# Kernel optimization log

Hardware: AMD Instinct MI355X
Metric: run time of the kernel (lower is better)

Reference implementation:

```python
import jax, jax.numpy as jnp
import numpy as np

N_NODES = 50000
N_EDGES = 1600000
N_GRAPHS = 500
BN_EPS = 1e-5


def gcn_conv(x, src, dst, W, b, n):
    # PyG GCNConv: add self-loops, symmetric normalization, scatter-add at target.
    xw = x @ W  # [N, out]
    deg = jax.ops.segment_sum(jnp.ones_like(dst, dtype=xw.dtype), dst, num_segments=n)
    dinv = jnp.where(deg > 0, jax.lax.rsqrt(deg), 0.0)
    coef = dinv[src] * dinv[dst]  # [E+N]
    out = jax.ops.segment_sum(xw[src] * coef[:, None], dst, num_segments=n)
    return out + b


def batchnorm(h, gamma, beta):
    # training-mode batch stats over the node dim (dropout omitted: eval)
    m = h.mean(axis=0)
    v = h.var(axis=0)
    return (h - m) * jax.lax.rsqrt(v + BN_EPS) * gamma + beta


def setup_inputs() -> dict:
    key = jax.random.key(0)
    ks = jax.random.split(key, 12)
    x = jax.random.normal(ks[0], (N_NODES, 64), dtype=jnp.float32)
    edge_index = jax.random.randint(ks[1], (2, N_EDGES), 0, N_NODES, dtype=jnp.int64)
    batch = jnp.sort(jax.random.randint(ks[2], (N_NODES,), 0, N_GRAPHS, dtype=jnp.int64))
    def glorot(k, shape):
        lim = float(np.sqrt(6.0 / (shape[0] + shape[1])))
        return jax.random.uniform(k, shape, jnp.float32, -lim, lim)
    return {
        "x": x, "edge_index": edge_index, "batch": batch,
        "W1": glorot(ks[3], (64, 128)), "b1": jnp.zeros((128,), jnp.float32),
        "gamma1": jnp.ones((128,), jnp.float32), "beta1": jnp.zeros((128,), jnp.float32),
        "W2": glorot(ks[4], (128, 128)), "b2": jnp.zeros((128,), jnp.float32),
        "gamma2": jnp.ones((128,), jnp.float32), "beta2": jnp.zeros((128,), jnp.float32),
        "W3": glorot(ks[5], (128, 256)), "b3": jnp.zeros((256,), jnp.float32),
        "gamma3": jnp.ones((256,), jnp.float32), "beta3": jnp.zeros((256,), jnp.float32),
        "W4": glorot(ks[6], (256, 10)), "b4": jnp.zeros((10,), jnp.float32),
    }


def reference(x, edge_index, batch, W1, b1, gamma1, beta1, W2, b2, gamma2, beta2,
              W3, b3, gamma3, beta3, W4, b4):
    n = x.shape[0]
    sl = jnp.arange(n, dtype=edge_index.dtype)
    src = jnp.concatenate([edge_index[0], sl])
    dst = jnp.concatenate([edge_index[1], sl])

    h = x
    for W, b, g, bt in ((W1, b1, gamma1, beta1), (W2, b2, gamma2, beta2)):
        h = gcn_conv(h, src, dst, W, b, n)
        h = jax.nn.relu(batchnorm(h, g, bt))

    # global mean pool over graphs
    sums = jax.ops.segment_sum(h, batch, num_segments=N_GRAPHS)
    cnts = jax.ops.segment_sum(jnp.ones((n,), h.dtype), batch, num_segments=N_GRAPHS)
    pooled = sums / jnp.maximum(cnts, 1.0)[:, None]  # [G, 128]

    # MLP head
    z = pooled @ W3 + b3
    z = jax.nn.relu(batchnorm(z, gamma3, beta3))
    return z @ W4 + b4  # [G, num_classes]
```

## Files before the change

kernel.cpp:

```cpp
#include <hip/hip_runtime.h>
#include <hip/hip_bf16.h>

#define BN_EPS 1e-5
#define PB 256

typedef __attribute__((ext_vector_type(8))) short short8;
typedef __attribute__((ext_vector_type(4))) float floatx4;


__device__ __forceinline__ unsigned short f2bf(float f) {
    union { float f; unsigned u; } v; v.f = f;
    unsigned r = v.u + 0x7FFF + ((v.u >> 16) & 1);
    return (unsigned short)(r >> 16);
}
__device__ __forceinline__ float bf2f(unsigned short h) {
    union { unsigned u; float f; } v; v.u = ((unsigned)h) << 16;
    return v.f;
}
__device__ __forceinline__ float lo16(unsigned u) { return bf2f((unsigned short)(u & 0xffff)); }
__device__ __forceinline__ float hi16(unsigned u) { return bf2f((unsigned short)(u >> 16)); }


__global__ void scan1_kernel(const int* __restrict__ in, int* __restrict__ part,
                             int* __restrict__ bsum, int n) {
    __shared__ int s[1024];
    int t = threadIdx.x;
    int i = blockIdx.x * 1024 + t;
    int v = (i < n) ? in[i] : 0;
    s[t] = v;
    __syncthreads();
    for (int off = 1; off < 1024; off <<= 1) {
        int x = (t >= off) ? s[t - off] : 0;
        __syncthreads();
        s[t] += x;
        __syncthreads();
    }
    if (i < n) part[i] = s[t] - v;
    if (t == 1023) bsum[blockIdx.x] = s[1023];
}

__global__ void scan2_kernel(int* __restrict__ bsum, int nb) {
    __shared__ int s[64];
    int t = threadIdx.x;
    int v = (t < nb) ? bsum[t] : 0;
    s[t] = v;
    __syncthreads();
    for (int off = 1; off < 64; off <<= 1) {
        int x = (t >= off) ? s[t - off] : 0;
        __syncthreads();
        s[t] += x;
        __syncthreads();
    }
    if (t < nb) bsum[t] = s[t] - v;
}

__global__ void scan3_rowptr(int* __restrict__ rowptr, const int* __restrict__ bsum,
                             int n, int E) {
    int i = blockIdx.x * blockDim.x + threadIdx.x;
    if (i < n) rowptr[i] += bsum[i >> 10];
    if (i == 0) rowptr[n] = E;
}

__global__ void scan3_add(int* __restrict__ arr, const int* __restrict__ bsum, int n) {
    int i = blockIdx.x * blockDim.x + threadIdx.x;
    if (i < n) arr[i] += bsum[i >> 10];
}


__global__ void hist_kernel(const int* __restrict__ dst, int* __restrict__ hist,
                            int E, int cpb, int NB) {
    __shared__ int h[256];
    int t = threadIdx.x;
    if (t < NB) h[t] = 0;
    __syncthreads();
    int base = blockIdx.x * cpb;
    int end = base + cpb; if (end > E) end = E;
    int e = base + t * 4;
    for (; e + 3 < end; e += 1024) {
        int4 d = *(const int4*)(dst + e);
        atomicAdd(&h[d.x >> 8], 1);
        atomicAdd(&h[d.y >> 8], 1);
        atomicAdd(&h[d.z >> 8], 1);
        atomicAdd(&h[d.w >> 8], 1);
    }
    for (; e < end; ++e) atomicAdd(&h[dst[e] >> 8], 1);
    __syncthreads();
    if (t < NB) hist[t * PB + blockIdx.x] = h[t];
}

__global__ void scatter_kernel(const int* __restrict__ src, const int* __restrict__ dst,
                               const int* __restrict__ offs, unsigned* __restrict__ part,
                               int E, int cpb, int NB) {
    __shared__ int cur[256];
    int t = threadIdx.x;
    if (t < NB) cur[t] = offs[t * PB + blockIdx.x];
    __syncthreads();
    int base = blockIdx.x * cpb;
    int end = base + cpb; if (end > E) end = E;
    int e = base + t * 4;
    for (; e + 3 < end; e += 1024) {
        int4 d4 = *(const int4*)(dst + e);
        int4 s4 = *(const int4*)(src + e);
        int dd[4] = {d4.x, d4.y, d4.z, d4.w};
        int sv[4] = {s4.x, s4.y, s4.z, s4.w};
#pragma unroll
        for (int i = 0; i < 4; ++i) {
            int pos = atomicAdd(&cur[dd[i] >> 8], 1);
            part[pos] = ((unsigned)sv[i] << 8) | (unsigned)(dd[i] & 255);
        }
    }
    for (; e < end; ++e) {
        int d = dst[e];
        int pos = atomicAdd(&cur[d >> 8], 1);
        part[pos] = ((unsigned)src[e] << 8) | (unsigned)(d & 255);
    }
}

__global__ void bucket_count(const unsigned* __restrict__ part, const int* __restrict__ offs,
                             int* __restrict__ cnt, float* __restrict__ dinv,
                             int E, int N, int NB) {
    __shared__ int cw[256];
    int b = blockIdx.x;
    int t = threadIdx.x;
    cw[t] = 0;
    __syncthreads();
    int bstart = offs[b * PB];
    int bend = (b + 1 < NB) ? offs[(b + 1) * PB] : E;
    for (int e = bstart + t; e < bend; e += 256)
        atomicAdd(&cw[part[e] & 255u], 1);
    __syncthreads();
    int node = (b << 8) + t;
    if (node < N) {
        int c = cw[t];
        cnt[node] = c;
        dinv[node] = rsqrtf((float)(c + 1));
    }
}

__global__ void bucket_fill(const unsigned* __restrict__ part, const int* __restrict__ offs,
                            const int* __restrict__ rowptr, int* __restrict__ csr,
                            int E, int N, int NB) {
    __shared__ int cur[256];
    int b = blockIdx.x;
    int t = threadIdx.x;
    int node = (b << 8) + t;
    cur[t] = (node < N) ? rowptr[node] : 0;
    __syncthreads();
    int bstart = offs[b * PB];
    int bend = (b + 1 < NB) ? offs[(b + 1) * PB] : E;
    for (int e = bstart + t; e < bend; e += 256) {
        unsigned pr = part[e];
        int pos = atomicAdd(&cur[pr & 255u], 1);
        csr[pos] = (int)(pr >> 8);
    }
}


__global__ void prescale64_bf(const float* __restrict__ x, const float* __restrict__ dinv,
                              unsigned short* __restrict__ y, int N) {
    int t = blockIdx.x * blockDim.x + threadIdx.x;
    int total = N * 8;
    if (t >= total) return;
    int r = t >> 3;
    float d = dinv[r];
    float4 a = ((const float4*)x)[t * 2];
    float4 b = ((const float4*)x)[t * 2 + 1];
    uint4 o;
    o.x = (unsigned)f2bf(a.x * d) | ((unsigned)f2bf(a.y * d) << 16);
    o.y = (unsigned)f2bf(a.z * d) | ((unsigned)f2bf(a.w * d) << 16);
    o.z = (unsigned)f2bf(b.x * d) | ((unsigned)f2bf(b.y * d) << 16);
    o.w = (unsigned)f2bf(b.z * d) | ((unsigned)f2bf(b.w * d) << 16);
    ((uint4*)y)[t] = o;
}

__global__ __launch_bounds__(256) void agg64_bf(
    const unsigned short* __restrict__ y, const int* __restrict__ rowptr,
    const int* __restrict__ csr, const float* __restrict__ dinv,
    unsigned short* __restrict__ A16, int N) {
    int wv = (blockIdx.x * blockDim.x + threadIdx.x) >> 6;
    int lane = threadIdx.x & 63;
    int node = wv * 2 + (lane >> 5);
    if (node >= N) return;
    int cu = lane & 31;
    const unsigned* yp = (const unsigned*)y;
    unsigned v = yp[(size_t)node * 32 + cu];
    float a0 = lo16(v), a1 = hi16(v);
    int b = rowptr[node], e = rowptr[node + 1];
    int i = b;
    for (; i + 7 < e; i += 8) {
        int s0 = csr[i], s1 = csr[i + 1], s2 = csr[i + 2], s3 = csr[i + 3];
        int s4 = csr[i + 4], s5 = csr[i + 5], s6 = csr[i + 6], s7 = csr[i + 7];
        unsigned v0 = yp[(size_t)s0 * 32 + cu];
        unsigned v1 = yp[(size_t)s1 * 32 + cu];
        unsigned v2 = yp[(size_t)s2 * 32 + cu];
        unsigned v3 = yp[(size_t)s3 * 32 + cu];
        unsigned v4 = yp[(size_t)s4 * 32 + cu];
        unsigned v5 = yp[(size_t)s5 * 32 + cu];
        unsigned v6 = yp[(size_t)s6 * 32 + cu];
        unsigned v7 = yp[(size_t)s7 * 32 + cu];
        a0 += ((lo16(v0) + lo16(v1)) + (lo16(v2) + lo16(v3)))
            + ((lo16(v4) + lo16(v5)) + (lo16(v6) + lo16(v7)));
        a1 += ((hi16(v0) + hi16(v1)) + (hi16(v2) + hi16(v3)))
            + ((hi16(v4) + hi16(v5)) + (hi16(v6) + hi16(v7)));
    }
    for (; i + 3 < e; i += 4) {
        int s0 = csr[i], s1 = csr[i + 1], s2 = csr[i + 2], s3 = csr[i + 3];
        unsigned v0 = yp[(size_t)s0 * 32 + cu];
        unsigned v1 = yp[(size_t)s1 * 32 + cu];
        unsigned v2 = yp[(size_t)s2 * 32 + cu];
        unsigned v3 = yp[(size_t)s3 * 32 + cu];
        a0 += (lo16(v0) + lo16(v1)) + (lo16(v2) + lo16(v3));
        a1 += (hi16(v0) + hi16(v1)) + (hi16(v2) + hi16(v3));
    }
    for (; i < e; ++i) {
        unsigned v0 = yp[(size_t)csr[i] * 32 + cu];
        a0 += lo16(v0);
        a1 += hi16(v0);
    }
    float d = dinv[node];
    ((unsigned*)A16)[(size_t)node * 32 + cu] =
        (unsigned)f2bf(a0 * d) | ((unsigned)f2bf(a1 * d) << 16);
}

__global__ __launch_bounds__(256) void agg128_bf(
    const unsigned short* __restrict__ y, const int* __restrict__ rowptr,
    const int* __restrict__ csr, const float* __restrict__ dinv,
    unsigned short* __restrict__ A16, int N) {
    int wv = (blockIdx.x * blockDim.x + threadIdx.x) >> 6;
    int lane = threadIdx.x & 63;
    int node = wv * 2 + (lane >> 5);
    if (node >= N) return;
    int c2 = lane & 31;
    const uint2* yp = (const uint2*)y;
    uint2 v = yp[(size_t)node * 32 + c2];
    float a0 = lo16(v.x), a1 = hi16(v.x), a2 = lo16(v.y), a3 = hi16(v.y);
    int b = rowptr[node], e = rowptr[node + 1];
    int i = b;
    for (; i + 7 < e; i += 8) {
        int s0 = csr[i], s1 = csr[i + 1], s2 = csr[i + 2], s3 = csr[i + 3];
        int s4 = csr[i + 4], s5 = csr[i + 5], s6 = csr[i + 6], s7 = csr[i + 7];
        uint2 v0 = yp[(size_t)s0 * 32 + c2];
        uint2 v1 = yp[(size_t)s1 * 32 + c2];
        uint2 v2 = yp[(size_t)s2 * 32 + c2];
        uint2 v3 = yp[(size_t)s3 * 32 + c2];
        uint2 v4 = yp[(size_t)s4 * 32 + c2];
        uint2 v5 = yp[(size_t)s5 * 32 + c2];
        uint2 v6 = yp[(size_t)s6 * 32 + c2];
        uint2 v7 = yp[(size_t)s7 * 32 + c2];
        a0 += ((lo16(v0.x) + lo16(v1.x)) + (lo16(v2.x) + lo16(v3.x)))
            + ((lo16(v4.x) + lo16(v5.x)) + (lo16(v6.x) + lo16(v7.x)));
        a1 += ((hi16(v0.x) + hi16(v1.x)) + (hi16(v2.x) + hi16(v3.x)))
            + ((hi16(v4.x) + hi16(v5.x)) + (hi16(v6.x) + hi16(v7.x)));
        a2 += ((lo16(v0.y) + lo16(v1.y)) + (lo16(v2.y) + lo16(v3.y)))
            + ((lo16(v4.y) + lo16(v5.y)) + (lo16(v6.y) + lo16(v7.y)));
        a3 += ((hi16(v0.y) + hi16(v1.y)) + (hi16(v2.y) + hi16(v3.y)))
            + ((hi16(v4.y) + hi16(v5.y)) + (hi16(v6.y) + hi16(v7.y)));
    }
    for (; i + 3 < e; i += 4) {
        int s0 = csr[i], s1 = csr[i + 1], s2 = csr[i + 2], s3 = csr[i + 3];
        uint2 v0 = yp[(size_t)s0 * 32 + c2];
        uint2 v1 = yp[(size_t)s1 * 32 + c2];
        uint2 v2 = yp[(size_t)s2 * 32 + c2];
        uint2 v3 = yp[(size_t)s3 * 32 + c2];
        a0 += (lo16(v0.x) + lo16(v1.x)) + (lo16(v2.x) + lo16(v3.x));
        a1 += (hi16(v0.x) + hi16(v1.x)) + (hi16(v2.x) + hi16(v3.x));
        a2 += (lo16(v0.y) + lo16(v1.y)) + (lo16(v2.y) + lo16(v3.y));
        a3 += (hi16(v0.y) + hi16(v1.y)) + (hi16(v2.y) + hi16(v3.y));
    }
    for (; i < e; ++i) {
        uint2 v0 = yp[(size_t)csr[i] * 32 + c2];
        a0 += lo16(v0.x);
        a1 += hi16(v0.x);
        a2 += lo16(v0.y);
        a3 += hi16(v0.y);
    }
    float d = dinv[node];
    uint2 o;
    o.x = (unsigned)f2bf(a0 * d) | ((unsigned)f2bf(a1 * d) << 16);
    o.y = (unsigned)f2bf(a2 * d) | ((unsigned)f2bf(a3 * d) << 16);
    ((uint2*)A16)[(size_t)node * 32 + c2] = o;
}

__global__ void wpack_kernel(const float* __restrict__ W, uint4* __restrict__ Wp, int K) {
    int i = blockIdx.x * blockDim.x + threadIdx.x;
    int total = K * 16;
    if (i >= total) return;
    int c = i & 127;
    int kb = i >> 7;
    unsigned short h[8];
#pragma unroll
    for (int j = 0; j < 8; ++j) h[j] = f2bf(W[(size_t)(kb * 8 + j) * 128 + c]);
    uint4 o;
    o.x = (unsigned)h[0] | ((unsigned)h[1] << 16);
    o.y = (unsigned)h[2] | ((unsigned)h[3] << 16);
    o.z = (unsigned)h[4] | ((unsigned)h[5] << 16);
    o.w = (unsigned)h[6] | ((unsigned)h[7] << 16);
    Wp[kb * 128 + c] = o;
}

template <int K>
__global__ __launch_bounds__(256) void mfma_gemm(const unsigned short* __restrict__ A16,
                                                 const uint4* __restrict__ Bp,
                                                 float* __restrict__ out,
                                                 double* __restrict__ st, int N) {
    constexpr int KS = K / 32;
    __shared__ float cs[128], cs2[128];
    if (threadIdx.x < 128) { cs[threadIdx.x] = 0.f; cs2[threadIdx.x] = 0.f; }
    int w = threadIdx.x >> 6, l = threadIdx.x & 63;
    int cl = l & 15, sub = l >> 4;
    int r0 = blockIdx.x * 64 + w * 16;
    int ra = r0 + cl; if (ra > N - 1) ra = N - 1;

    short8 a[KS];
    const unsigned short* ap = A16 + (size_t)ra * K + sub * 8;
#pragma unroll
    for (int ks = 0; ks < KS; ++ks) a[ks] = *(const short8*)(ap + ks * 32);

    floatx4 acc[8] = {};
#pragma unroll
    for (int cb = 0; cb < 8; ++cb) {
#pragma unroll
        for (int ks = 0; ks < KS; ++ks) {
            short8 b = *(const short8*)&Bp[(ks * 4 + sub) * 128 + cb * 16 + cl];
            acc[cb] = __builtin_amdgcn_mfma_f32_16x16x32_bf16(a[ks], b, acc[cb], 0, 0, 0);
        }
    }
    __syncthreads();
#pragma unroll
    for (int cb = 0; cb < 8; ++cb) {
        float s = 0.f, s2 = 0.f;
#pragma unroll
        for (int j = 0; j < 4; ++j) {
            int row = r0 + sub * 4 + j;
            if (row < N) {
                float val = acc[cb][j];
                out[(size_t)row * 128 + cb * 16 + cl] = val;
                s += val;
                s2 += val * val;
            }
        }
        atomicAdd(&cs[cb * 16 + cl], s);
        atomicAdd(&cs2[cb * 16 + cl], s2);
    }
    __syncthreads();
    if (threadIdx.x < 128) {
        atomicAdd(&st[threadIdx.x], (double)cs[threadIdx.x]);
        atomicAdd(&st[128 + threadIdx.x], (double)cs2[threadIdx.x]);
    }
}

__global__ void colstats_kernel(const float* __restrict__ h, int N, int C, int logC,
                                double* __restrict__ st) {
    int c = threadIdx.x & (C - 1);
    int sub = threadIdx.x >> logC;
    int rpb = 256 >> logC;
    float s = 0.f, s2 = 0.f;
    for (int r = blockIdx.x * rpb + sub; r < N; r += gridDim.x * rpb) {
        float v = h[(size_t)r * C + c];
        s += v;
        s2 += v * v;
    }
    atomicAdd(&st[c], (double)s);
    atomicAdd(&st[C + c], (double)s2);
}

__global__ void bnfin_kernel(const double* __restrict__ st, const float* __restrict__ gamma,
                             const float* __restrict__ beta, float2* __restrict__ ss,
                             int N, int C) {
    int c = blockIdx.x * blockDim.x + threadIdx.x;
    if (c >= C) return;
    double mean = st[c] / N;
    double var = st[C + c] / N - mean * mean;
    float sc = (float)((double)gamma[c] / sqrt(var + BN_EPS));
    float sh = beta[c] - (float)mean * sc;
    ss[c] = make_float2(sc, sh);
}

__global__ void normrelu_bf(const float* __restrict__ h, const float2* __restrict__ ss,
                            const float* __restrict__ dinv, unsigned short* __restrict__ out,
                            int N) {
    int t = blockIdx.x * blockDim.x + threadIdx.x;
    int total = N * 16;
    if (t >= total) return;
    int r = t >> 4;
    int j = (t & 15) << 3;
    float d = dinv[r];
    float4 a = ((const float4*)h)[t * 2];
    float4 b = ((const float4*)h)[t * 2 + 1];
    float2 s0 = ss[j], s1 = ss[j + 1], s2 = ss[j + 2], s3 = ss[j + 3];
    float2 s4 = ss[j + 4], s5 = ss[j + 5], s6 = ss[j + 6], s7 = ss[j + 7];
    float v0 = fmaxf(a.x * s0.x + s0.y, 0.f) * d;
    float v1 = fmaxf(a.y * s1.x + s1.y, 0.f) * d;
    float v2 = fmaxf(a.z * s2.x + s2.y, 0.f) * d;
    float v3 = fmaxf(a.w * s3.x + s3.y, 0.f) * d;
    float v4 = fmaxf(b.x * s4.x + s4.y, 0.f) * d;
    float v5 = fmaxf(b.y * s5.x + s5.y, 0.f) * d;
    float v6 = fmaxf(b.z * s6.x + s6.y, 0.f) * d;
    float v7 = fmaxf(b.w * s7.x + s7.y, 0.f) * d;
    uint4 o;
    o.x = (unsigned)f2bf(v0) | ((unsigned)f2bf(v1) << 16);
    o.y = (unsigned)f2bf(v2) | ((unsigned)f2bf(v3) << 16);
    o.z = (unsigned)f2bf(v4) | ((unsigned)f2bf(v5) << 16);
    o.w = (unsigned)f2bf(v6) | ((unsigned)f2bf(v7) << 16);
    ((uint4*)out)[t] = o;
}

__global__ void bounds_kernel(const int* __restrict__ batch, int* __restrict__ gstart,
                              int N, int G) {
    int i = blockIdx.x * blockDim.x + threadIdx.x;
    if (i >= N) return;
    int bi = batch[i];
    int bp = (i == 0) ? -1 : batch[i - 1];
    for (int g = bp + 1; g <= bi; ++g) gstart[g] = i;
    if (i == N - 1) {
        for (int g = bi + 1; g <= G; ++g) gstart[g] = N;
    }
}

__global__ void pool_bn_kernel(const float* __restrict__ h, const float2* __restrict__ ss,
                               const int* __restrict__ gstart, float* __restrict__ pooled) {
    int g = blockIdx.x;
    int c = threadIdx.x;
    float2 sc = ss[c];
    int b = gstart[g], e = gstart[g + 1];
    float acc = 0.f;
    int r = b;
    for (; r + 1 < e; r += 2) {
        float v0 = h[(size_t)r * 128 + c];
        float v1 = h[(size_t)(r + 1) * 128 + c];
        acc += fmaxf(v0 * sc.x + sc.y, 0.f) + fmaxf(v1 * sc.x + sc.y, 0.f);
    }
    if (r < e) acc += fmaxf(h[(size_t)r * 128 + c] * sc.x + sc.y, 0.f);
    pooled[(size_t)g * 128 + c] = acc / fmaxf((float)(e - b), 1.0f);
}

template <int K>
__global__ __launch_bounds__(256) void gemm_bias_kernel(const float* __restrict__ A,
                                                        const float* __restrict__ W,
                                                        const float* __restrict__ bias,
                                                        float* __restrict__ out, int N, int C) {
    __shared__ float Wl[K * 128];
    const int ct = blockIdx.y << 7;
    for (int idx = threadIdx.x; idx < K * 128; idx += 256) {
        int kk = idx >> 7, cc = idx & 127;
        Wl[idx] = W[(size_t)kk * C + ct + cc];
    }
    __syncthreads();
    const int cq = (threadIdx.x & 31) << 2;
    const int rg = threadIdx.x >> 5;
    const int r0 = blockIdx.x * 32 + (rg << 2);

    const float* Ap[4];
#pragma unroll
    for (int i = 0; i < 4; ++i) {
        int r = r0 + i;
        Ap[i] = A + (size_t)(r < N ? r : 0) * K;
    }
    float acc[4][4] = {};
#pragma unroll 4
    for (int k = 0; k < K; ++k) {
        float a0 = Ap[0][k];
        float a1 = Ap[1][k];
        float a2 = Ap[2][k];
        float a3 = Ap[3][k];
        float4 w = *(const float4*)&Wl[k * 128 + cq];
        acc[0][0] += a0 * w.x; acc[0][1] += a0 * w.y; acc[0][2] += a0 * w.z; acc[0][3] += a0 * w.w;
        acc[1][0] += a1 * w.x; acc[1][1] += a1 * w.y; acc[1][2] += a1 * w.z; acc[1][3] += a1 * w.w;
        acc[2][0] += a2 * w.x; acc[2][1] += a2 * w.y; acc[2][2] += a2 * w.z; acc[2][3] += a2 * w.w;
        acc[3][0] += a3 * w.x; acc[3][1] += a3 * w.y; acc[3][2] += a3 * w.z; acc[3][3] += a3 * w.w;
    }
    float4 bv = *(const float4*)&bias[ct + cq];
#pragma unroll
    for (int i = 0; i < 4; ++i) {
        int r = r0 + i;
        if (r < N) {
            float4 o = make_float4(acc[i][0] + bv.x, acc[i][1] + bv.y,
                                   acc[i][2] + bv.z, acc[i][3] + bv.w);
            *(float4*)&out[(size_t)r * C + ct + cq] = o;
        }
    }
}

__global__ void head_kernel(const float* __restrict__ z, const float2* __restrict__ ss,
                            const float* __restrict__ W4, const float* __restrict__ b4,
                            float* __restrict__ out, int G) {
    __shared__ float zr[256];
    int g = blockIdx.x;
    int t = threadIdx.x;
    float v = z[(size_t)g * 256 + t];
    zr[t] = fmaxf(v * ss[t].x + ss[t].y, 0.f);
    __syncthreads();
    int j = t >> 4;
    int part = t & 15;
    if (j < 10) {
        float acc = 0.f;
#pragma unroll
        for (int k = 0; k < 16; ++k) {
            int c = part + k * 16;
            acc += zr[c] * W4[c * 10 + j];
        }
#pragma unroll
        for (int off = 8; off; off >>= 1) acc += __shfl_down(acc, off);
        if (part == 0) out[(size_t)g * 10 + j] = acc + b4[j];
    }
}


extern "C" void kernel_launch(void* const* d_in, const int* in_sizes, int n_in,
                              void* d_out, int out_size, void* d_ws, size_t ws_size,
                              hipStream_t stream) {
    const int N = in_sizes[0] / 64;
    const int E = in_sizes[1] / 2;
    const int G = out_size / 10;

    const float* x     = (const float*)d_in[0];
    const int*   ei    = (const int*)d_in[1];
    const int*   batch = (const int*)d_in[2];
    const float* W1 = (const float*)d_in[3];
    const float* g1 = (const float*)d_in[5];
    const float* be1 = (const float*)d_in[6];
    const float* W2 = (const float*)d_in[7];
    const float* g2 = (const float*)d_in[9];
    const float* be2 = (const float*)d_in[10];
    const float* W3 = (const float*)d_in[11];
    const float* b3 = (const float*)d_in[12];
    const float* g3 = (const float*)d_in[13];
    const float* be3 = (const float*)d_in[14];
    const float* W4 = (const float*)d_in[15];
    const float* b4 = (const float*)d_in[16];
    float* out = (float*)d_out;

    const int* srcp = ei;
    const int* dstp = ei + E;

    char* p = (char*)d_ws;
    auto alloc = [&](size_t bytes) {
        void* r = (void*)p;
        p += (bytes + 255) & ~(size_t)255;
        return r;
    };
    unsigned short* A16 = (unsigned short*)alloc((size_t)N * 128 * 2);
    float* Bb = (float*)alloc((size_t)N * 128 * 4);
    char* R3  = (char*)alloc((size_t)N * 128 * 4);
    int* csr      = (int*)alloc((size_t)E * 4);
    unsigned* part = (unsigned*)alloc((size_t)E * 4);
    int* cnt    = (int*)alloc((size_t)N * 4);
    int* rowptr = (int*)alloc((size_t)(N + 1) * 4);
    float* dinv = (float*)alloc((size_t)N * 4);
    int* hist   = (int*)alloc((size_t)256 * PB * 4);
    int* offs   = (int*)alloc((size_t)256 * PB * 4);
    int* bsums  = (int*)alloc(64 * 4);
    uint4* w1p  = (uint4*)alloc((size_t)64 * 128 * 2);
    uint4* w2p  = (uint4*)alloc((size_t)128 * 128 * 2);
    int* gstart = (int*)alloc((size_t)(G + 1) * 4);
    float* pooled = (float*)alloc((size_t)G * 128 * 4);
    float* z      = (float*)alloc((size_t)G * 256 * 4);
    double* st    = (double*)alloc(1024 * 8);
    float2* ss    = (float2*)alloc(512 * 8);
    (void)ws_size; (void)n_in;

    unsigned short* c16 = (unsigned short*)R3;
    unsigned short* y16 = (unsigned short*)(R3 + (size_t)N * 128 * 2);

    double* stA = st;
    double* stB = st + 256;
    double* stC = st + 512;
    float2* ssA = ss;
    float2* ssB = ss + 128;
    float2* ssC = ss + 256;

    hipMemsetAsync(st, 0, 1024 * 8, stream);

    const int nb = (N + 255) / 256;
    const int nchunks = (N + 1023) / 1024;
    const int NB = (N + 255) >> 8;
    const int cpb = (((E + PB - 1) / PB) + 3) & ~3;
    const int n2 = NB * PB;
    const int nch2 = (n2 + 1023) / 1024;
    const int aggblocks = (N + 7) / 8;

    wpack_kernel<<<4, 256, 0, stream>>>(W1, w1p, 64);
    wpack_kernel<<<8, 256, 0, stream>>>(W2, w2p, 128);

    hist_kernel<<<PB, 256, 0, stream>>>(dstp, hist, E, cpb, NB);
    scan1_kernel<<<nch2, 1024, 0, stream>>>(hist, offs, bsums, n2);
    scan2_kernel<<<1, 64, 0, stream>>>(bsums, nch2);
    scan3_add<<<(n2 + 255) / 256, 256, 0, stream>>>(offs, bsums, n2);
    scatter_kernel<<<PB, 256, 0, stream>>>(srcp, dstp, offs, part, E, cpb, NB);

    bucket_count<<<NB, 256, 0, stream>>>(part, offs, cnt, dinv, E, N, NB);

    scan1_kernel<<<nchunks, 1024, 0, stream>>>(cnt, rowptr, bsums, N);
    scan2_kernel<<<1, 64, 0, stream>>>(bsums, nchunks);
    scan3_rowptr<<<nb, 256, 0, stream>>>(rowptr, bsums, N, E);
    bucket_fill<<<NB, 256, 0, stream>>>(part, offs, rowptr, csr, E, N, NB);

    prescale64_bf<<<(N * 8 + 255) / 256, 256, 0, stream>>>(x, dinv, y16, N);
    agg64_bf<<<aggblocks, 256, 0, stream>>>(y16, rowptr, csr, dinv, A16, N);
    mfma_gemm<64><<<(N + 63) / 64, 256, 0, stream>>>(A16, w1p, Bb, stA, N);
    bnfin_kernel<<<1, 128, 0, stream>>>(stA, g1, be1, ssA, N, 128);
    normrelu_bf<<<(N * 16 + 255) / 256, 256, 0, stream>>>(Bb, ssA, dinv, c16, N);

    agg128_bf<<<aggblocks, 256, 0, stream>>>(c16, rowptr, csr, dinv, A16, N);
    mfma_gemm<128><<<(N + 63) / 64, 256, 0, stream>>>(A16, w2p, Bb, stB, N);
    bnfin_kernel<<<1, 128, 0, stream>>>(stB, g2, be2, ssB, N, 128);

    bounds_kernel<<<nb, 256, 0, stream>>>(batch, gstart, N, G);
    pool_bn_kernel<<<G, 128, 0, stream>>>(Bb, ssB, gstart, pooled);

    gemm_bias_kernel<128><<<dim3((G + 31) / 32, 2), 256, 0, stream>>>(pooled, W3, b3, z, G, 256);
    colstats_kernel<<<64, 256, 0, stream>>>(z, G, 256, 8, stC);
    bnfin_kernel<<<1, 256, 0, stream>>>(stC, g3, be3, ssC, G, 256);
    head_kernel<<<G, 256, 0, stream>>>(z, ssC, W4, b4, out, G);
}
```

Measured before the change: 272.4 us.

## Fuse scan passes, derive rowptr per bucket, prefetch CSR indices in aggregation

Merges the second and third prefix-scan stages into one kernel that re-scans block sums in shared memory. It also computes rowptr directly inside the bucket count kernel with a local scan offset by the bucket start, which drops the separate node-level scan chain. Together these remove four kernel launches and the cnt buffer. The aggregation kernels now software-pipeline CSR index loads one batch ahead using nontemporal loads, hiding index latency behind the gathers at the cost of extra registers.

Result: no change. 270.6 us (-0.7%).

```diff
diff --git a/kernel.cpp b/kernel.cpp
--- a/kernel.cpp
+++ b/kernel.cpp
@@ -39,31 +39,24 @@
     if (t == 1023) bsum[blockIdx.x] = s[1023];
 }
 
-__global__ void scan2_kernel(int* __restrict__ bsum, int nb) {
+__global__ void scan23_add(int* __restrict__ arr, const int* __restrict__ bsum,
+                           int nb, int n) {
     __shared__ int s[64];
     int t = threadIdx.x;
-    int v = (t < nb) ? bsum[t] : 0;
-    s[t] = v;
+    if (t < 64) s[t] = (t < nb) ? bsum[t] : 0;
     __syncthreads();
     for (int off = 1; off < 64; off <<= 1) {
-        int x = (t >= off) ? s[t - off] : 0;
+        int x = (t < 64 && t >= off) ? s[t - off] : 0;
         __syncthreads();
-        s[t] += x;
+        if (t < 64) s[t] += x;
         __syncthreads();
     }
-    if (t < nb) bsum[t] = s[t] - v;
-}
-
-__global__ void scan3_rowptr(int* __restrict__ rowptr, const int* __restrict__ bsum,
-                             int n, int E) {
-    int i = blockIdx.x * blockDim.x + threadIdx.x;
-    if (i < n) rowptr[i] += bsum[i >> 10];
-    if (i == 0) rowptr[n] = E;
-}
-
-__global__ void scan3_add(int* __restrict__ arr, const int* __restrict__ bsum, int n) {
-    int i = blockIdx.x * blockDim.x + threadIdx.x;
-    if (i < n) arr[i] += bsum[i >> 10];
+    int i = blockIdx.x * blockDim.x + t;
+    if (i < n) {
+        int ch = i >> 10;
+        int pre = (ch == 0) ? 0 : s[ch - 1];
+        arr[i] += pre;
+    }
 }
 
 
@@ -116,10 +109,10 @@
     }
 }
 
-__global__ void bucket_count(const unsigned* __restrict__ part, const int* __restrict__ offs,
-                             int* __restrict__ cnt, float* __restrict__ dinv,
-                             int E, int N, int NB) {
-    __shared__ int cw[256];
+__global__ void bucket_rowptr(const unsigned* __restrict__ part, const int* __restrict__ offs,
+                              int* __restrict__ rowptr, float* __restrict__ dinv,
+                              int E, int N, int NB) {
+    __shared__ int cw[256], sc[256];
     int b = blockIdx.x;
     int t = threadIdx.x;
     cw[t] = 0;
@@ -129,12 +122,21 @@
     for (int e = bstart + t; e < bend; e += 256)
         atomicAdd(&cw[part[e] & 255u], 1);
     __syncthreads();
+    int c = cw[t];
+    sc[t] = c;
+    __syncthreads();
+    for (int off = 1; off < 256; off <<= 1) {
+        int x = (t >= off) ? sc[t - off] : 0;
+        __syncthreads();
+        sc[t] += x;
+        __syncthreads();
+    }
     int node = (b << 8) + t;
     if (node < N) {
-        int c = cw[t];
-        cnt[node] = c;
+        rowptr[node] = bstart + sc[t] - c;
         dinv[node] = rsqrtf((float)(c + 1));
     }
+    if (b == NB - 1 && t == 255) rowptr[N] = E;
 }
 
 __global__ void bucket_fill(const unsigned* __restrict__ part, const int* __restrict__ offs,
@@ -187,24 +189,60 @@
     float a0 = lo16(v), a1 = hi16(v);
     int b = rowptr[node], e = rowptr[node + 1];
     int i = b;
-    for (; i + 7 < e; i += 8) {
-        int s0 = csr[i], s1 = csr[i + 1], s2 = csr[i + 2], s3 = csr[i + 3];
-        int s4 = csr[i + 4], s5 = csr[i + 5], s6 = csr[i + 6], s7 = csr[i + 7];
-        unsigned v0 = yp[(size_t)s0 * 32 + cu];
-        unsigned v1 = yp[(size_t)s1 * 32 + cu];
-        unsigned v2 = yp[(size_t)s2 * 32 + cu];
-        unsigned v3 = yp[(size_t)s3 * 32 + cu];
-        unsigned v4 = yp[(size_t)s4 * 32 + cu];
-        unsigned v5 = yp[(size_t)s5 * 32 + cu];
-        unsigned v6 = yp[(size_t)s6 * 32 + cu];
-        unsigned v7 = yp[(size_t)s7 * 32 + cu];
+    int n0, n1, n2, n3, n4, n5, n6, n7;
+    if (i + 7 < e) {
+        n0 = __builtin_nontemporal_load(csr + i);
+        n1 = __builtin_nontemporal_load(csr + i + 1);
+        n2 = __builtin_nontemporal_load(csr + i + 2);
+        n3 = __builtin_nontemporal_load(csr + i + 3);
+        n4 = __builtin_nontemporal_load(csr + i + 4);
+        n5 = __builtin_nontemporal_load(csr + i + 5);
+        n6 = __builtin_nontemporal_load(csr + i + 6);
+        n7 = __builtin_nontemporal_load(csr + i + 7);
+    }
+    for (; i + 15 < e; i += 8) {
+        int c0 = n0, c1 = n1, c2 = n2, c3 = n3, c4 = n4, c5 = n5, c6 = n6, c7 = n7;
+        n0 = __builtin_nontemporal_load(csr + i + 8);
+        n1 = __builtin_nontemporal_load(csr + i + 9);
+        n2 = __builtin_nontemporal_load(csr + i + 10);
+        n3 = __builtin_nontemporal_load(csr + i + 11);
+        n4 = __builtin_nontemporal_load(csr + i + 12);
+        n5 = __builtin_nontemporal_load(csr + i + 13);
+        n6 = __builtin_nontemporal_load(csr + i + 14);
+        n7 = __builtin_nontemporal_load(csr + i + 15);
+        unsigned v0 = yp[(size_t)c0 * 32 + cu];
+        unsigned v1 = yp[(size_t)c1 * 32 + cu];
+        unsigned v2 = yp[(size_t)c2 * 32 + cu];
+        unsigned v3 = yp[(size_t)c3 * 32 + cu];
+        unsigned v4 = yp[(size_t)c4 * 32 + cu];
+        unsigned v5 = yp[(size_t)c5 * 32 + cu];
+        unsigned v6 = yp[(size_t)c6 * 32 + cu];
+        unsigned v7 = yp[(size_t)c7 * 32 + cu];
         a0 += ((lo16(v0) + lo16(v1)) + (lo16(v2) + lo16(v3)))
             + ((lo16(v4) + lo16(v5)) + (lo16(v6) + lo16(v7)));
         a1 += ((hi16(v0) + hi16(v1)) + (hi16(v2) + hi16(v3)))
             + ((hi16(v4) + hi16(v5)) + (hi16(v6) + hi16(v7)));
     }
+    if (i + 7 < e) {
+        unsigned v0 = yp[(size_t)n0 * 32 + cu];
+        unsigned v1 = yp[(size_t)n1 * 32 + cu];
+        unsigned v2 = yp[(size_t)n2 * 32 + cu];
+        unsigned v3 = yp[(size_t)n3 * 32 + cu];
+        unsigned v4 = yp[(size_t)n4 * 32 + cu];
+        unsigned v5 = yp[(size_t)n5 * 32 + cu];
+        unsigned v6 = yp[(size_t)n6 * 32 + cu];
+        unsigned v7 = yp[(size_t)n7 * 32 + cu];
+        a0 += ((lo16(v0) + lo16(v1)) + (lo16(v2) + lo16(v3)))
+            + ((lo16(v4) + lo16(v5)) + (lo16(v6) + lo16(v7)));
+        a1 += ((hi16(v0) + hi16(v1)) + (hi16(v2) + hi16(v3)))
+            + ((hi16(v4) + hi16(v5)) + (hi16(v6) + hi16(v7)));
+        i += 8;
+    }
     for (; i + 3 < e; i += 4) {
-        int s0 = csr[i], s1 = csr[i + 1], s2 = csr[i + 2], s3 = csr[i + 3];
+        int s0 = __builtin_nontemporal_load(csr + i);
+        int s1 = __builtin_nontemporal_load(csr + i + 1);
+        int s2 = __builtin_nontemporal_load(csr + i + 2);
+        int s3 = __builtin_nontemporal_load(csr + i + 3);
         unsigned v0 = yp[(size_t)s0 * 32 + cu];
         unsigned v1 = yp[(size_t)s1 * 32 + cu];
         unsigned v2 = yp[(size_t)s2 * 32 + cu];
@@ -213,7 +251,7 @@
         a1 += (hi16(v0) + hi16(v1)) + (hi16(v2) + hi16(v3));
     }
     for (; i < e; ++i) {
-        unsigned v0 = yp[(size_t)csr[i] * 32 + cu];
+        unsigned v0 = yp[(size_t)__builtin_nontemporal_load(csr + i) * 32 + cu];
         a0 += lo16(v0);
         a1 += hi16(v0);
     }
@@ -236,17 +274,35 @@
     float a0 = lo16(v.x), a1 = hi16(v.x), a2 = lo16(v.y), a3 = hi16(v.y);
     int b = rowptr[node], e = rowptr[node + 1];
     int i = b;
-    for (; i + 7 < e; i += 8) {
-        int s0 = csr[i], s1 = csr[i + 1], s2 = csr[i + 2], s3 = csr[i + 3];
-        int s4 = csr[i + 4], s5 = csr[i + 5], s6 = csr[i + 6], s7 = csr[i + 7];
-        uint2 v0 = yp[(size_t)s0 * 32 + c2];
-        uint2 v1 = yp[(size_t)s1 * 32 + c2];
-        uint2 v2 = yp[(size_t)s2 * 32 + c2];
-        uint2 v3 = yp[(size_t)s3 * 32 + c2];
-        uint2 v4 = yp[(size_t)s4 * 32 + c2];
-        uint2 v5 = yp[(size_t)s5 * 32 + c2];
-        uint2 v6 = yp[(size_t)s6 * 32 + c2];
-        uint2 v7 = yp[(size_t)s7 * 32 + c2];
+    int n0, n1, n2, n3, n4, n5, n6, n7;
+    if (i + 7 < e) {
+        n0 = __builtin_nontemporal_load(csr + i);
+        n1 = __builtin_nontemporal_load(csr + i + 1);
+        n2 = __builtin_nontemporal_load(csr + i + 2);
+        n3 = __builtin_nontemporal_load(csr + i + 3);
+        n4 = __builtin_nontemporal_load(csr + i + 4);
+        n5 = __builtin_nontemporal_load(csr + i + 5);
+        n6 = __builtin_nontemporal_load(csr + i + 6);
+        n7 = __builtin_nontemporal_load(csr + i + 7);
+    }
+    for (; i + 15 < e; i += 8) {
+        int c0 = n0, c1 = n1, c2i = n2, c3 = n3, c4 = n4, c5 = n5, c6 = n6, c7 = n7;
+        n0 = __builtin_nontemporal_load(csr + i + 8);
+        n1 = __builtin_nontemporal_load(csr + i + 9);
+        n2 = __builtin_nontemporal_load(csr + i + 10);
+        n3 = __builtin_nontemporal_load(csr + i + 11);
+        n4 = __builtin_nontemporal_load(csr + i + 12);
+        n5 = __builtin_nontemporal_load(csr + i + 13);
+        n6 = __builtin_nontemporal_load(csr + i + 14);
+        n7 = __builtin_nontemporal_load(csr + i + 15);
+        uint2 v0 = yp[(size_t)c0 * 32 + c2];
+        uint2 v1 = yp[(size_t)c1 * 32 + c2];
+        uint2 v2 = yp[(size_t)c2i * 32 + c2];
+        uint2 v3 = yp[(size_t)c3 * 32 + c2];
+        uint2 v4 = yp[(size_t)c4 * 32 + c2];
+        uint2 v5 = yp[(size_t)c5 * 32 + c2];
+        uint2 v6 = yp[(size_t)c6 * 32 + c2];
+        uint2 v7 = yp[(size_t)c7 * 32 + c2];
         a0 += ((lo16(v0.x) + lo16(v1.x)) + (lo16(v2.x) + lo16(v3.x)))
             + ((lo16(v4.x) + lo16(v5.x)) + (lo16(v6.x) + lo16(v7.x)));
         a1 += ((hi16(v0.x) + hi16(v1.x)) + (hi16(v2.x) + hi16(v3.x)))
@@ -256,8 +312,30 @@
         a3 += ((hi16(v0.y) + hi16(v1.y)) + (hi16(v2.y) + hi16(v3.y)))
             + ((hi16(v4.y) + hi16(v5.y)) + (hi16(v6.y) + hi16(v7.y)));
     }
+    if (i + 7 < e) {
+        uint2 v0 = yp[(size_t)n0 * 32 + c2];
+        uint2 v1 = yp[(size_t)n1 * 32 + c2];
+        uint2 v2 = yp[(size_t)n2 * 32 + c2];
+        uint2 v3 = yp[(size_t)n3 * 32 + c2];
+        uint2 v4 = yp[(size_t)n4 * 32 + c2];
+        uint2 v5 = yp[(size_t)n5 * 32 + c2];
+        uint2 v6 = yp[(size_t)n6 * 32 + c2];
+        uint2 v7 = yp[(size_t)n7 * 32 + c2];
+        a0 += ((lo16(v0.x) + lo16(v1.x)) + (lo16(v2.x) + lo16(v3.x)))
+            + ((lo16(v4.x) + lo16(v5.x)) + (lo16(v6.x) + lo16(v7.x)));
+        a1 += ((hi16(v0.x) + hi16(v1.x)) + (hi16(v2.x) + hi16(v3.x)))
+            + ((hi16(v4.x) + hi16(v5.x)) + (hi16(v6.x) + hi16(v7.x)));
+        a2 += ((lo16(v0.y) + lo16(v1.y)) + (lo16(v2.y) + lo16(v3.y)))
+            + ((lo16(v4.y) + lo16(v5.y)) + (lo16(v6.y) + lo16(v7.y)));
+        a3 += ((hi16(v0.y) + hi16(v1.y)) + (hi16(v2.y) + hi16(v3.y)))
+            + ((hi16(v4.y) + hi16(v5.y)) + (hi16(v6.y) + hi16(v7.y)));
+        i += 8;
+    }
     for (; i + 3 < e; i += 4) {
-        int s0 = csr[i], s1 = csr[i + 1], s2 = csr[i + 2], s3 = csr[i + 3];
+        int s0 = __builtin_nontemporal_load(csr + i);
+        int s1 = __builtin_nontemporal_load(csr + i + 1);
+        int s2 = __builtin_nontemporal_load(csr + i + 2);
+        int s3 = __builtin_nontemporal_load(csr + i + 3);
         uint2 v0 = yp[(size_t)s0 * 32 + c2];
         uint2 v1 = yp[(size_t)s1 * 32 + c2];
         uint2 v2 = yp[(size_t)s2 * 32 + c2];
@@ -268,7 +346,7 @@
         a3 += (hi16(v0.y) + hi16(v1.y)) + (hi16(v2.y) + hi16(v3.y));
     }
     for (; i < e; ++i) {
-        uint2 v0 = yp[(size_t)csr[i] * 32 + c2];
+        uint2 v0 = yp[(size_t)__builtin_nontemporal_load(csr + i) * 32 + c2];
         a0 += lo16(v0.x);
         a1 += hi16(v0.x);
         a2 += lo16(v0.y);
@@ -544,7 +622,6 @@
     char* R3  = (char*)alloc((size_t)N * 128 * 4);
     int* csr      = (int*)alloc((size_t)E * 4);
     unsigned* part = (unsigned*)alloc((size_t)E * 4);
-    int* cnt    = (int*)alloc((size_t)N * 4);
     int* rowptr = (int*)alloc((size_t)(N + 1) * 4);
     float* dinv = (float*)alloc((size_t)N * 4);
     int* hist   = (int*)alloc((size_t)256 * PB * 4);
@@ -572,7 +649,6 @@
     hipMemsetAsync(st, 0, 1024 * 8, stream);
 
     const int nb = (N + 255) / 256;
-    const int nchunks = (N + 1023) / 1024;
     const int NB = (N + 255) >> 8;
     const int cpb = (((E + PB - 1) / PB) + 3) & ~3;
     const int n2 = NB * PB;
@@ -584,15 +660,10 @@
 
     hist_kernel<<<PB, 256, 0, stream>>>(dstp, hist, E, cpb, NB);
     scan1_kernel<<<nch2, 1024, 0, stream>>>(hist, offs, bsums, n2);
-    scan2_kernel<<<1, 64, 0, stream>>>(bsums, nch2);
-    scan3_add<<<(n2 + 255) / 256, 256, 0, stream>>>(offs, bsums, n2);
+    scan23_add<<<(n2 + 255) / 256, 256, 0, stream>>>(offs, bsums, nch2, n2);
     scatter_kernel<<<PB, 256, 0, stream>>>(srcp, dstp, offs, part, E, cpb, NB);
 
-    bucket_count<<<NB, 256, 0, stream>>>(part, offs, cnt, dinv, E, N, NB);
-
-    scan1_kernel<<<nchunks, 1024, 0, stream>>>(cnt, rowptr, bsums, N);
-    scan2_kernel<<<1, 64, 0, stream>>>(bsums, nchunks);
-    scan3_rowptr<<<nb, 256, 0, stream>>>(rowptr, bsums, N, E);
+    bucket_rowptr<<<NB, 256, 0, stream>>>(part, offs, rowptr, dinv, E, N, NB);
     bucket_fill<<<NB, 256, 0, stream>>>(part, offs, rowptr, csr, E, N, NB);
 
     prescale64_bf<<<(N * 8 + 255) / 256, 256, 0, stream>>>(x, dinv, y16, N);
```

## Fuse scan, rowptr, BN finalize and colstats kernels; store GEMM output in bf16

Applied to the files above, without the earlier changes.

Merges scan2 and scan3 into one kernel and computes rowptr directly in each bucket with a local scan, which drops the separate cnt array and its three-kernel scan. The BN finalize steps are folded into the consumer kernels (normrelu, pool, head), and the head GEMM now accumulates column stats itself, so bnfin and colstats launches go away. The GCN GEMM output is stored as bf16 instead of fp32, halving that write and its reread while the stats are still taken from fp32 values. Launch overhead drops, at the cost of bf16 rounding on pre-BN activations and some redundant finalize math in every block.

Result: faster. 255.9 us (-6.1%).

```diff
diff --git a/kernel.cpp b/kernel.cpp
--- a/kernel.cpp
+++ b/kernel.cpp
@@ -39,31 +39,24 @@
     if (t == 1023) bsum[blockIdx.x] = s[1023];
 }
 
-__global__ void scan2_kernel(int* __restrict__ bsum, int nb) {
+__global__ void scan23_add(int* __restrict__ arr, const int* __restrict__ bsum,
+                           int nb, int n) {
     __shared__ int s[64];
     int t = threadIdx.x;
-    int v = (t < nb) ? bsum[t] : 0;
-    s[t] = v;
+    if (t < 64) s[t] = (t < nb) ? bsum[t] : 0;
     __syncthreads();
     for (int off = 1; off < 64; off <<= 1) {
-        int x = (t >= off) ? s[t - off] : 0;
+        int x = (t < 64 && t >= off) ? s[t - off] : 0;
         __syncthreads();
-        s[t] += x;
+        if (t < 64) s[t] += x;
         __syncthreads();
     }
-    if (t < nb) bsum[t] = s[t] - v;
-}
-
-__global__ void scan3_rowptr(int* __restrict__ rowptr, const int* __restrict__ bsum,
-                             int n, int E) {
-    int i = blockIdx.x * blockDim.x + threadIdx.x;
-    if (i < n) rowptr[i] += bsum[i >> 10];
-    if (i == 0) rowptr[n] = E;
-}
-
-__global__ void scan3_add(int* __restrict__ arr, const int* __restrict__ bsum, int n) {
-    int i = blockIdx.x * blockDim.x + threadIdx.x;
-    if (i < n) arr[i] += bsum[i >> 10];
+    int i = blockIdx.x * blockDim.x + t;
+    if (i < n) {
+        int ch = i >> 10;
+        int pre = (ch == 0) ? 0 : s[ch - 1];
+        arr[i] += pre;
+    }
 }
 
 
@@ -116,10 +109,10 @@
     }
 }
 
-__global__ void bucket_count(const unsigned* __restrict__ part, const int* __restrict__ offs,
-                             int* __restrict__ cnt, float* __restrict__ dinv,
-                             int E, int N, int NB) {
-    __shared__ int cw[256];
+__global__ void bucket_rowptr(const unsigned* __restrict__ part, const int* __restrict__ offs,
+                              int* __restrict__ rowptr, float* __restrict__ dinv,
+                              int E, int N, int NB) {
+    __shared__ int cw[256], sc[256];
     int b = blockIdx.x;
     int t = threadIdx.x;
     cw[t] = 0;
@@ -129,12 +122,21 @@
     for (int e = bstart + t; e < bend; e += 256)
         atomicAdd(&cw[part[e] & 255u], 1);
     __syncthreads();
+    int c = cw[t];
+    sc[t] = c;
+    __syncthreads();
+    for (int off = 1; off < 256; off <<= 1) {
+        int x = (t >= off) ? sc[t - off] : 0;
+        __syncthreads();
+        sc[t] += x;
+        __syncthreads();
+    }
     int node = (b << 8) + t;
     if (node < N) {
-        int c = cw[t];
-        cnt[node] = c;
+        rowptr[node] = bstart + sc[t] - c;
         dinv[node] = rsqrtf((float)(c + 1));
     }
+    if (b == NB - 1 && t == 255) rowptr[N] = E;
 }
 
 __global__ void bucket_fill(const unsigned* __restrict__ part, const int* __restrict__ offs,
@@ -301,7 +303,7 @@
 template <int K>
 __global__ __launch_bounds__(256) void mfma_gemm(const unsigned short* __restrict__ A16,
                                                  const uint4* __restrict__ Bp,
-                                                 float* __restrict__ out,
+                                                 unsigned short* __restrict__ out16,
                                                  double* __restrict__ st, int N) {
     constexpr int KS = K / 32;
     __shared__ float cs[128], cs2[128];
@@ -334,7 +336,7 @@
             int row = r0 + sub * 4 + j;
             if (row < N) {
                 float val = acc[cb][j];
-                out[(size_t)row * 128 + cb * 16 + cl] = val;
+                out16[(size_t)row * 128 + cb * 16 + cl] = f2bf(val);
                 s += val;
                 s2 += val * val;
             }
@@ -349,54 +351,37 @@
     }
 }
 
-__global__ void colstats_kernel(const float* __restrict__ h, int N, int C, int logC,
-                                double* __restrict__ st) {
-    int c = threadIdx.x & (C - 1);
-    int sub = threadIdx.x >> logC;
-    int rpb = 256 >> logC;
-    float s = 0.f, s2 = 0.f;
-    for (int r = blockIdx.x * rpb + sub; r < N; r += gridDim.x * rpb) {
-        float v = h[(size_t)r * C + c];
-        s += v;
-        s2 += v * v;
-    }
-    atomicAdd(&st[c], (double)s);
-    atomicAdd(&st[C + c], (double)s2);
-}
-
-__global__ void bnfin_kernel(const double* __restrict__ st, const float* __restrict__ gamma,
-                             const float* __restrict__ beta, float2* __restrict__ ss,
-                             int N, int C) {
-    int c = blockIdx.x * blockDim.x + threadIdx.x;
-    if (c >= C) return;
-    double mean = st[c] / N;
-    double var = st[C + c] / N - mean * mean;
-    float sc = (float)((double)gamma[c] / sqrt(var + BN_EPS));
-    float sh = beta[c] - (float)mean * sc;
-    ss[c] = make_float2(sc, sh);
-}
-
-__global__ void normrelu_bf(const float* __restrict__ h, const float2* __restrict__ ss,
-                            const float* __restrict__ dinv, unsigned short* __restrict__ out,
-                            int N) {
+__global__ __launch_bounds__(256) void normrelu_bf(
+    const unsigned short* __restrict__ h16, const double* __restrict__ st,
+    const float* __restrict__ gamma, const float* __restrict__ beta,
+    const float* __restrict__ dinv, unsigned short* __restrict__ out, int N) {
+    __shared__ float2 ssl[128];
+    if (threadIdx.x < 128) {
+        int c = threadIdx.x;
+        double mean = st[c] / N;
+        double var = st[128 + c] / N - mean * mean;
+        float sc = (float)((double)gamma[c] / sqrt(var + BN_EPS));
+        float sh = beta[c] - (float)mean * sc;
+        ssl[c] = make_float2(sc, sh);
+    }
+    __syncthreads();
     int t = blockIdx.x * blockDim.x + threadIdx.x;
     int total = N * 16;
     if (t >= total) return;
     int r = t >> 4;
     int j = (t & 15) << 3;
     float d = dinv[r];
-    float4 a = ((const float4*)h)[t * 2];
-    float4 b = ((const float4*)h)[t * 2 + 1];
-    float2 s0 = ss[j], s1 = ss[j + 1], s2 = ss[j + 2], s3 = ss[j + 3];
-    float2 s4 = ss[j + 4], s5 = ss[j + 5], s6 = ss[j + 6], s7 = ss[j + 7];
-    float v0 = fmaxf(a.x * s0.x + s0.y, 0.f) * d;
-    float v1 = fmaxf(a.y * s1.x + s1.y, 0.f) * d;
-    float v2 = fmaxf(a.z * s2.x + s2.y, 0.f) * d;
-    float v3 = fmaxf(a.w * s3.x + s3.y, 0.f) * d;
-    float v4 = fmaxf(b.x * s4.x + s4.y, 0.f) * d;
-    float v5 = fmaxf(b.y * s5.x + s5.y, 0.f) * d;
-    float v6 = fmaxf(b.z * s6.x + s6.y, 0.f) * d;
-    float v7 = fmaxf(b.w * s7.x + s7.y, 0.f) * d;
+    uint4 hv = ((const uint4*)h16)[t];
+    float2 s0 = ssl[j], s1 = ssl[j + 1], s2 = ssl[j + 2], s3 = ssl[j + 3];
+    float2 s4 = ssl[j + 4], s5 = ssl[j + 5], s6 = ssl[j + 6], s7 = ssl[j + 7];
+    float v0 = fmaxf(lo16(hv.x) * s0.x + s0.y, 0.f) * d;
+    float v1 = fmaxf(hi16(hv.x) * s1.x + s1.y, 0.f) * d;
+    float v2 = fmaxf(lo16(hv.y) * s2.x + s2.y, 0.f) * d;
+    float v3 = fmaxf(hi16(hv.y) * s3.x + s3.y, 0.f) * d;
+    float v4 = fmaxf(lo16(hv.z) * s4.x + s4.y, 0.f) * d;
+    float v5 = fmaxf(hi16(hv.z) * s5.x + s5.y, 0.f) * d;
+    float v6 = fmaxf(lo16(hv.w) * s6.x + s6.y, 0.f) * d;
+    float v7 = fmaxf(hi16(hv.w) * s7.x + s7.y, 0.f) * d;
     uint4 o;
     o.x = (unsigned)f2bf(v0) | ((unsigned)f2bf(v1) << 16);
     o.y = (unsigned)f2bf(v2) | ((unsigned)f2bf(v3) << 16);
@@ -417,29 +402,39 @@
     }
 }
 
-__global__ void pool_bn_kernel(const float* __restrict__ h, const float2* __restrict__ ss,
-                               const int* __restrict__ gstart, float* __restrict__ pooled) {
+__global__ void pool_bn_kernel(const unsigned short* __restrict__ h16,
+                               const double* __restrict__ st,
+                               const float* __restrict__ gamma, const float* __restrict__ beta,
+                               const int* __restrict__ gstart, float* __restrict__ pooled,
+                               int N) {
     int g = blockIdx.x;
     int c = threadIdx.x;
-    float2 sc = ss[c];
+    double mean = st[c] / N;
+    double var = st[128 + c] / N - mean * mean;
+    float sc = (float)((double)gamma[c] / sqrt(var + BN_EPS));
+    float sh = beta[c] - (float)mean * sc;
     int b = gstart[g], e = gstart[g + 1];
     float acc = 0.f;
     int r = b;
     for (; r + 1 < e; r += 2) {
-        float v0 = h[(size_t)r * 128 + c];
-        float v1 = h[(size_t)(r + 1) * 128 + c];
-        acc += fmaxf(v0 * sc.x + sc.y, 0.f) + fmaxf(v1 * sc.x + sc.y, 0.f);
-    }
-    if (r < e) acc += fmaxf(h[(size_t)r * 128 + c] * sc.x + sc.y, 0.f);
+        float v0 = bf2f(h16[(size_t)r * 128 + c]);
+        float v1 = bf2f(h16[(size_t)(r + 1) * 128 + c]);
+        acc += fmaxf(v0 * sc + sh, 0.f) + fmaxf(v1 * sc + sh, 0.f);
+    }
+    if (r < e) acc += fmaxf(bf2f(h16[(size_t)r * 128 + c]) * sc + sh, 0.f);
     pooled[(size_t)g * 128 + c] = acc / fmaxf((float)(e - b), 1.0f);
 }
 
 template <int K>
-__global__ __launch_bounds__(256) void gemm_bias_kernel(const float* __restrict__ A,
-                                                        const float* __restrict__ W,
-                                                        const float* __restrict__ bias,
-                                                        float* __restrict__ out, int N, int C) {
+__global__ __launch_bounds__(256) void gemm_bias_stats(const float* __restrict__ A,
+                                                       const float* __restrict__ W,
+                                                       const float* __restrict__ bias,
+                                                       float* __restrict__ out,
+                                                       double* __restrict__ st,
+                                                       int N, int C) {
     __shared__ float Wl[K * 128];
+    __shared__ float cs[128], cs2[128];
+    if (threadIdx.x < 128) { cs[threadIdx.x] = 0.f; cs2[threadIdx.x] = 0.f; }
     const int ct = blockIdx.y << 7;
     for (int idx = threadIdx.x; idx < K * 128; idx += 256) {
         int kk = idx >> 7, cc = idx & 127;
@@ -470,25 +465,45 @@
         acc[3][0] += a3 * w.x; acc[3][1] += a3 * w.y; acc[3][2] += a3 * w.z; acc[3][3] += a3 * w.w;
     }
     float4 bv = *(const float4*)&bias[ct + cq];
+    float s[4] = {}, s2[4] = {};
 #pragma unroll
     for (int i = 0; i < 4; ++i) {
         int r = r0 + i;
         if (r < N) {
-            float4 o = make_float4(acc[i][0] + bv.x, acc[i][1] + bv.y,
-                                   acc[i][2] + bv.z, acc[i][3] + bv.w);
-            *(float4*)&out[(size_t)r * C + ct + cq] = o;
+            float o0 = acc[i][0] + bv.x, o1 = acc[i][1] + bv.y;
+            float o2 = acc[i][2] + bv.z, o3 = acc[i][3] + bv.w;
+            *(float4*)&out[(size_t)r * C + ct + cq] = make_float4(o0, o1, o2, o3);
+            s[0] += o0; s2[0] += o0 * o0;
+            s[1] += o1; s2[1] += o1 * o1;
+            s[2] += o2; s2[2] += o2 * o2;
+            s[3] += o3; s2[3] += o3 * o3;
         }
     }
-}
-
-__global__ void head_kernel(const float* __restrict__ z, const float2* __restrict__ ss,
+#pragma unroll
+    for (int jj = 0; jj < 4; ++jj) {
+        atomicAdd(&cs[cq + jj], s[jj]);
+        atomicAdd(&cs2[cq + jj], s2[jj]);
+    }
+    __syncthreads();
+    if (threadIdx.x < 128) {
+        atomicAdd(&st[ct + threadIdx.x], (double)cs[threadIdx.x]);
+        atomicAdd(&st[C + ct + threadIdx.x], (double)cs2[threadIdx.x]);
+    }
+}
+
+__global__ void head_kernel(const float* __restrict__ z, const double* __restrict__ st,
+                            const float* __restrict__ gamma, const float* __restrict__ beta,
                             const float* __restrict__ W4, const float* __restrict__ b4,
                             float* __restrict__ out, int G) {
     __shared__ float zr[256];
     int g = blockIdx.x;
     int t = threadIdx.x;
+    double mean = st[t] / G;
+    double var = st[256 + t] / G - mean * mean;
+    float sc = (float)((double)gamma[t] / sqrt(var + BN_EPS));
+    float sh = beta[t] - (float)mean * sc;
     float v = z[(size_t)g * 256 + t];
-    zr[t] = fmaxf(v * ss[t].x + ss[t].y, 0.f);
+    zr[t] = fmaxf(v * sc + sh, 0.f);
     __syncthreads();
     int j = t >> 4;
     int part = t & 15;
@@ -540,11 +555,10 @@
         return r;
     };
     unsigned short* A16 = (unsigned short*)alloc((size_t)N * 128 * 2);
-    float* Bb = (float*)alloc((size_t)N * 128 * 4);
+    unsigned short* h16 = (unsigned short*)alloc((size_t)N * 128 * 2);
     char* R3  = (char*)alloc((size_t)N * 128 * 4);
     int* csr      = (int*)alloc((size_t)E * 4);
     unsigned* part = (unsigned*)alloc((size_t)E * 4);
-    int* cnt    = (int*)alloc((size_t)N * 4);
     int* rowptr = (int*)alloc((size_t)(N + 1) * 4);
     float* dinv = (float*)alloc((size_t)N * 4);
     int* hist   = (int*)alloc((size_t)256 * PB * 4);
@@ -556,7 +570,6 @@
     float* pooled = (float*)alloc((size_t)G * 128 * 4);
     float* z      = (float*)alloc((size_t)G * 256 * 4);
     double* st    = (double*)alloc(1024 * 8);
-    float2* ss    = (float2*)alloc(512 * 8);
     (void)ws_size; (void)n_in;
 
     unsigned short* c16 = (unsigned short*)R3;
@@ -565,14 +578,10 @@
     double* stA = st;
     double* stB = st + 256;
     double* stC = st + 512;
-    float2* ssA = ss;
-    float2* ssB = ss + 128;
-    float2* ssC = ss + 256;
 
     hipMemsetAsync(st, 0, 1024 * 8, stream);
 
     const int nb = (N + 255) / 256;
-    const int nchunks = (N + 1023) / 1024;
     const int NB = (N + 255) >> 8;
     const int cpb = (((E + PB - 1) / PB) + 3) & ~3;
     const int n2 = NB * PB;
@@ -584,32 +593,23 @@
 
     hist_kernel<<<PB, 256, 0, stream>>>(dstp, hist, E, cpb, NB);
     scan1_kernel<<<nch2, 1024, 0, stream>>>(hist, offs, bsums, n2);
-    scan2_kernel<<<1, 64, 0, stream>>>(bsums, nch2);
-    scan3_add<<<(n2 + 255) / 256, 256, 0, stream>>>(offs, bsums, n2);
+    scan23_add<<<(n2 + 255) / 256, 256, 0, stream>>>(offs, bsums, nch2, n2);
     scatter_kernel<<<PB, 256, 0, stream>>>(srcp, dstp, offs, part, E, cpb, NB);
 
-    bucket_count<<<NB, 256, 0, stream>>>(part, offs, cnt, dinv, E, N, NB);
-
-    scan1_kernel<<<nchunks, 1024, 0, stream>>>(cnt, rowptr, bsums, N);
-    scan2_kernel<<<1, 64, 0, stream>>>(bsums, nchunks);
-    scan3_rowptr<<<nb, 256, 0, stream>>>(rowptr, bsums, N, E);
+    bucket_rowptr<<<NB, 256, 0, stream>>>(part, offs, rowptr, dinv, E, N, NB);
     bucket_fill<<<NB, 256, 0, stream>>>(part, offs, rowptr, csr, E, N, NB);
 
     prescale64_bf<<<(N * 8 + 255) / 256, 256, 0, stream>>>(x, dinv, y16, N);
     agg64_bf<<<aggblocks, 256, 0, stream>>>(y16, rowptr, csr, dinv, A16, N);
-    mfma_gemm<64><<<(N + 63) / 64, 256, 0, stream>>>(A16, w1p, Bb, stA, N);
-    bnfin_kernel<<<1, 128, 0, stream>>>(stA, g1, be1, ssA, N, 128);
-    normrelu_bf<<<(N * 16 + 255) / 256, 256, 0, stream>>>(Bb, ssA, dinv, c16, N);
+    mfma_gemm<64><<<(N + 63) / 64, 256, 0, stream>>>(A16, w1p, h16, stA, N);
+    normrelu_bf<<<(N * 16 + 255) / 256, 256, 0, stream>>>(h16, stA, g1, be1, dinv, c16, N);
 
     agg128_bf<<<aggblocks, 256, 0, stream>>>(c16, rowptr, csr, dinv, A16, N);
-    mfma_gemm<128><<<(N + 63) / 64, 256, 0, stream>>>(A16, w2p, Bb, stB, N);
-    bnfin_kernel<<<1, 128, 0, stream>>>(stB, g2, be2, ssB, N, 128);
+    mfma_gemm<128><<<(N + 63) / 64, 256, 0, stream>>>(A16, w2p, h16, stB, N);
 
     bounds_kernel<<<nb, 256, 0, stream>>>(batch, gstart, N, G);
-    pool_bn_kernel<<<G, 128, 0, stream>>>(Bb, ssB, gstart, pooled);
-
-    gemm_bias_kernel<128><<<dim3((G + 31) / 32, 2), 256, 0, stream>>>(pooled, W3, b3, z, G, 256);
-    colstats_kernel<<<64, 256, 0, stream>>>(z, G, 256, 8, stC);
-    bnfin_kernel<<<1, 256, 0, stream>>>(stC, g3, be3, ssC, G, 256);
-    head_kernel<<<G, 256, 0, stream>>>(z, ssC, W4, b4, out, G);
-}
+    pool_bn_kernel<<<G, 128, 0, stream>>>(h16, stB, g2, be2, gstart, pooled, N);
+
+    gemm_bias_stats<128><<<dim3((G + 31) / 32, 2), 256, 0, stream>>>(pooled, W3, b3, z, stC, G, 256);
+    head_kernel<<<G, 256, 0, stream>>>(z, stC, g3, be3, W4, b4, out, G);
+}
```
